# Optimization experiments

Hardware: AMD Instinct MI355X
Metric: run time of the kernel (lower is better)

## Reference

```python
import jax, jax.numpy as jnp
import numpy as np

N_NODES = 100000
N_EDGES = 1600000
IN_FEATS = 256
OUT_FEATS = 128


def setup_inputs() -> dict:
    key = jax.random.key(0)
    k1, k2, k3, k4, k5 = jax.random.split(key, 5)
    feat = jax.random.normal(k1, (N_NODES, IN_FEATS), dtype=jnp.float32)
    # xavier_uniform-like init for the weight
    limit = float(np.sqrt(6.0 / (IN_FEATS + OUT_FEATS)))
    weight = jax.random.uniform(k2, (IN_FEATS, OUT_FEATS), dtype=jnp.float32,
                                minval=-limit, maxval=limit)
    edge_weight = jax.random.uniform(k3, (N_EDGES,), dtype=jnp.float32)
    src = jax.random.randint(k4, (N_EDGES,), 0, N_NODES, dtype=jnp.int64)
    dst = jax.random.randint(k5, (N_EDGES,), 0, N_NODES, dtype=jnp.int64)
    return {"feat": feat, "weight": weight, "edge_weight": edge_weight,
            "src": src, "dst": dst}


def reference(feat, weight, edge_weight, src, dst):
    N = feat.shape[0]
    ones = jnp.ones(src.shape, dtype=feat.dtype)
    # out/in degrees from edge list (clamped to >= 1), as in DGL
    out_deg = jnp.clip(jax.ops.segment_sum(ones, src, num_segments=N), 1.0)
    in_deg = jnp.clip(jax.ops.segment_sum(ones, dst, num_segments=N), 1.0)
    # norm == 'both': pre-scale sources by out_deg^-0.5
    feat_src = feat * (out_deg ** -0.5)[:, None]
    # in_feats > out_feats branch: transform (with tanh) BEFORE aggregation
    h = jnp.tanh(feat_src @ weight)                      # [N, out]
    # message = u_mul_e: h[src] * edge_weight, then sum per destination
    m = h[src] * edge_weight[:, None]                    # [E, out]
    rst = jax.ops.segment_sum(m, dst, num_segments=N)    # [N, out]
    # norm == 'both': post-scale by in_deg^-0.5
    rst = rst * (in_deg ** -0.5)[:, None]
    return rst
```

## Files before the change

kernel.cpp:

```cpp
#include <hip/hip_runtime.h>
#include <hip/hip_fp16.h>
#include <math.h>

#define N_NODES 100000
#define N_EDGES 1600000
#define IN_F 256
#define OUT_F 128
#define SCAN_TPB 256
#define SCAN_EPB 1024

#define HR 4
#define HRANGE 25000
#define HC 64
#define HCHUNK 25000
#define PWORDS (N_NODES / 2)

#define GM_ROWS 64
#define BK 32

typedef _Float16 h8 __attribute__((ext_vector_type(8)));
typedef float f4 __attribute__((ext_vector_type(4)));
typedef int   i4v __attribute__((ext_vector_type(4)));
typedef int   i2v __attribute__((ext_vector_type(2)));
typedef float f4v __attribute__((ext_vector_type(4)));

#define GLD16(gp, lp) __builtin_amdgcn_global_load_lds( \
    (const __attribute__((address_space(1))) unsigned int*)(gp), \
    (__attribute__((address_space(3))) unsigned int*)(lp), 16, 0, 0)

__global__ __launch_bounds__(256) void hist_kernel(
        const int* __restrict__ src, const int* __restrict__ dst,
        int* __restrict__ rank, unsigned int* __restrict__ partial_in,
        unsigned int* __restrict__ partial_out) {
    __shared__ unsigned int bins[HRANGE / 2];
    int b = blockIdx.x;
    int c = b >> 3;
    int tr = b & 7;
    int type = tr >> 2;
    int r = tr & 3;
    for (int i = threadIdx.x; i < HRANGE / 2; i += 256) bins[i] = 0;
    __syncthreads();
    const int* nodes = type ? src : dst;
    const int e0 = c * HCHUNK;
    const int lo = r * HRANGE;
    const int ngroups = HCHUNK / 4;
    for (int g = threadIdx.x; g < ngroups; g += 256) {
        int e = e0 + g * 4;
        int4 n4 = *(const int4*)(nodes + e);
        int nn[4] = {n4.x, n4.y, n4.z, n4.w};
        #pragma unroll
        for (int j = 0; j < 4; ++j) {
            unsigned loc = (unsigned)(nn[j] - lo);
            if (loc < (unsigned)HRANGE) {
                unsigned sh = (loc & 1) * 16;
                unsigned old = atomicAdd(&bins[loc >> 1], 1u << sh);
                if (type == 0) rank[e + j] = (int)((old >> sh) & 0xffffu);
            }
        }
    }
    __syncthreads();
    unsigned int* part = type ? partial_out : partial_in;
    unsigned int* dstp = part + (size_t)c * PWORDS + (lo >> 1);
    for (int i = threadIdx.x; i < HRANGE / 2; i += 256) dstp[i] = bins[i];
}

__global__ __launch_bounds__(256) void fused_reduce_kernel(
        const unsigned int* __restrict__ partial_in,
        const unsigned int* __restrict__ partial_out,
        unsigned short* __restrict__ chunk_base16,
        int* __restrict__ deg_in, float* __restrict__ rs_out,
        int* __restrict__ spart, int N) {
    __shared__ int tmp[256];
    int t = threadIdx.x;
    int n0 = blockIdx.x * SCAN_EPB + t * 4;
    int run[4] = {0, 0, 0, 0};
    int sout[4] = {0, 0, 0, 0};
    if (n0 < N) {
        const int w0 = n0 >> 1;
        #pragma unroll 4
        for (int c = 0; c < HC; ++c) {
            ushort4 cb;
            cb.x = (unsigned short)run[0]; cb.y = (unsigned short)run[1];
            cb.z = (unsigned short)run[2]; cb.w = (unsigned short)run[3];
            *(ushort4*)(chunk_base16 + (size_t)c * N_NODES + n0) = cb;
            uint2 pi = *(const uint2*)(partial_in + (size_t)c * PWORDS + w0);
            run[0] += (int)(pi.x & 0xffffu);  run[1] += (int)(pi.x >> 16);
            run[2] += (int)(pi.y & 0xffffu);  run[3] += (int)(pi.y >> 16);
            uint2 po = *(const uint2*)(partial_out + (size_t)c * PWORDS + w0);
            sout[0] += (int)(po.x & 0xffffu); sout[1] += (int)(po.x >> 16);
            sout[2] += (int)(po.y & 0xffffu); sout[3] += (int)(po.y >> 16);
        }
        *(int4*)(deg_in + n0) = make_int4(run[0], run[1], run[2], run[3]);
        float4 rs;
        rs.x = rsqrtf((float)(sout[0] < 1 ? 1 : sout[0]));
        rs.y = rsqrtf((float)(sout[1] < 1 ? 1 : sout[1]));
        rs.z = rsqrtf((float)(sout[2] < 1 ? 1 : sout[2]));
        rs.w = rsqrtf((float)(sout[3] < 1 ? 1 : sout[3]));
        *(float4*)(rs_out + n0) = rs;
    }
    tmp[t] = run[0] + run[1] + run[2] + run[3];
    __syncthreads();
    for (int off = 128; off > 0; off >>= 1) {
        if (t < off) tmp[t] += tmp[t + off];
        __syncthreads();
    }
    if (t == 0) spart[blockIdx.x] = tmp[0];
}

__global__ __launch_bounds__(128) void scan_part2(const int* __restrict__ partials,
                                                  int* __restrict__ bases, int nb) {
    __shared__ int tmp[128];
    int t = threadIdx.x;
    int v = (t < nb) ? partials[t] : 0;
    tmp[t] = v;
    __syncthreads();
    int x = v;
    for (int off = 1; off < 128; off <<= 1) {
        int y = (t >= off) ? tmp[t - off] : 0;
        __syncthreads();
        x += y;
        tmp[t] = x;
        __syncthreads();
    }
    if (t < nb) bases[t] = x - v;
}

__global__ __launch_bounds__(SCAN_TPB) void scan_part3(const int* __restrict__ deg,
                                                       const int* __restrict__ bases,
                                                       int* __restrict__ row_ptr, int N) {
    __shared__ int tmp[SCAN_TPB];
    int t = threadIdx.x;
    int i0 = blockIdx.x * SCAN_EPB + t * 4;
    int v[4];
    int s = 0;
    #pragma unroll
    for (int j = 0; j < 4; ++j) { v[j] = (i0 + j < N) ? deg[i0 + j] : 0; s += v[j]; }
    tmp[t] = s;
    __syncthreads();
    int x = s;
    for (int off = 1; off < SCAN_TPB; off <<= 1) {
        int y = (t >= off) ? tmp[t - off] : 0;
        __syncthreads();
        x += y;
        tmp[t] = x;
        __syncthreads();
    }
    int excl = bases[blockIdx.x] + x - s;
    #pragma unroll
    for (int j = 0; j < 4; ++j) {
        if (i0 + j < N) row_ptr[i0 + j] = excl;
        excl += v[j];
    }
    if (blockIdx.x == gridDim.x - 1 && t == SCAN_TPB - 1) row_ptr[N] = bases[blockIdx.x] + x;
}

__global__ __launch_bounds__(256) void fill_kernel(
        const int* __restrict__ src, const int* __restrict__ dst,
        const float* __restrict__ ew, const int* __restrict__ row_ptr,
        const unsigned short* __restrict__ chunk_base16,
        const int* __restrict__ rank, int2* __restrict__ ed, int E) {
    int e0 = (blockIdx.x * 256 + threadIdx.x) * 4;
    if (e0 >= E) return;
    i4v s4 = __builtin_nontemporal_load((const i4v*)(src + e0));
    i4v d4 = __builtin_nontemporal_load((const i4v*)(dst + e0));
    f4v w4 = __builtin_nontemporal_load((const f4v*)(ew + e0));
    i4v r4 = __builtin_nontemporal_load((const i4v*)(rank + e0));
    int c = e0 / HCHUNK;
    const unsigned short* cb = chunk_base16 + (size_t)c * N_NODES;
    #pragma unroll
    for (int j = 0; j < 4; ++j) {
        int d = d4[j];
        int p = row_ptr[d] + (int)cb[d] + r4[j];
        unsigned long long v = (unsigned long long)(unsigned int)s4[j] |
                               ((unsigned long long)(unsigned int)__float_as_int(w4[j]) << 32);
        __builtin_nontemporal_store(v, (unsigned long long*)&ed[p]);
    }
}

__global__ void wt_kernel(const float* __restrict__ W, _Float16* __restrict__ Wt) {
    int i = blockIdx.x * blockDim.x + threadIdx.x;
    if (i < IN_F * OUT_F) {
        int n = i >> 8;
        int k = i & 255;
        Wt[i] = (_Float16)W[k * OUT_F + n];
    }
}

__device__ __forceinline__ float fast_tanh(float x) {
    float e = __expf(2.0f * x);
    return 1.0f - 2.0f / (e + 1.0f);
}

__global__ __launch_bounds__(256, 4) void gemm_mfma_kernel(
        const float* __restrict__ feat, const _Float16* __restrict__ Wt,
        const float* __restrict__ rs_out, __half* __restrict__ h, int N) {
    __shared__ float    a_lds[2][GM_ROWS * BK];
    __shared__ _Float16 b_lds[2][OUT_F * BK];

    const int tid  = threadIdx.x;
    const int wave = tid >> 6;
    const int lane = tid & 63;
    const int m    = lane & 15;
    const int quad = lane >> 4;
    const int n0   = wave * 32;
    const int r0   = blockIdx.x * GM_ROWS;

    const int l3 = lane >> 3;
    const int ag = (lane & 7) ^ l3;
    int arow0 = r0 + 16 * wave + l3;      if (arow0 >= N) arow0 = N - 1;
    int arow1 = r0 + 16 * wave + 8 + l3;  if (arow1 >= N) arow1 = N - 1;
    const float* ga0 = feat + (size_t)arow0 * IN_F + ag * 4;
    const float* ga1 = feat + (size_t)arow1 * IN_F + ag * 4;
    const int brow0 = 32 * wave + (lane >> 2);
    const int brow1 = 32 * wave + 16 + (lane >> 2);
    const _Float16* gb0 = Wt + (size_t)brow0 * IN_F + (lane & 3) * 8;
    const _Float16* gb1 = Wt + (size_t)brow1 * IN_F + (lane & 3) * 8;

    f4 acc[4][2];
    #pragma unroll
    for (int t = 0; t < 4; ++t) {
        acc[t][0] = (f4){0.f, 0.f, 0.f, 0.f};
        acc[t][1] = (f4){0.f, 0.f, 0.f, 0.f};
    }

    GLD16(ga0, &a_lds[0][(16 * wave) * BK]);
    GLD16(ga1, &a_lds[0][(16 * wave + 8) * BK]);
    GLD16(gb0, &b_lds[0][(32 * wave) * BK]);
    GLD16(gb1, &b_lds[0][(32 * wave + 16) * BK]);
    __syncthreads();

    #pragma unroll
    for (int kt = 0; kt < IN_F / BK; ++kt) {
        const int cb = kt & 1;
        if (kt < IN_F / BK - 1) {
            const int nb2 = cb ^ 1;
            const int ko = (kt + 1) * BK;
            GLD16(ga0 + ko, &a_lds[nb2][(16 * wave) * BK]);
            GLD16(ga1 + ko, &a_lds[nb2][(16 * wave + 8) * BK]);
            GLD16(gb0 + ko, &b_lds[nb2][(32 * wave) * BK]);
            GLD16(gb1 + ko, &b_lds[nb2][(32 * wave + 16) * BK]);
            __builtin_amdgcn_sched_barrier(0);
        }
        h8 b0 = *(const h8*)&b_lds[cb][(n0 + m) * BK + quad * 8];
        h8 b1 = *(const h8*)&b_lds[cb][(n0 + 16 + m) * BK + quad * 8];
        #pragma unroll
        for (int t = 0; t < 4; ++t) {
            const int ar = t * 16 + m;
            float4 alo = *(const float4*)&a_lds[cb][ar * BK + (((quad * 2)     ^ (m & 7)) * 4)];
            float4 ahi = *(const float4*)&a_lds[cb][ar * BK + (((quad * 2 + 1) ^ (m & 7)) * 4)];
            h8 a;
            a[0] = (_Float16)alo.x; a[1] = (_Float16)alo.y;
            a[2] = (_Float16)alo.z; a[3] = (_Float16)alo.w;
            a[4] = (_Float16)ahi.x; a[5] = (_Float16)ahi.y;
            a[6] = (_Float16)ahi.z; a[7] = (_Float16)ahi.w;
            acc[t][0] = __builtin_amdgcn_mfma_f32_16x16x32_f16(a, b0, acc[t][0], 0, 0, 0);
            acc[t][1] = __builtin_amdgcn_mfma_f32_16x16x32_f16(a, b1, acc[t][1], 0, 0, 0);
        }
        __syncthreads();
    }

    #pragma unroll
    for (int t = 0; t < 4; ++t) {
        const int crow = r0 + t * 16 + quad * 4;
        float4 rs4 = *(const float4*)&rs_out[crow];
        const float rsv[4] = {rs4.x, rs4.y, rs4.z, rs4.w};
        #pragma unroll
        for (int r = 0; r < 4; ++r) {
            const int rr = crow + r;
            if (rr < N) {
                h[(size_t)rr * OUT_F + n0 + m]      = __float2half(fast_tanh(acc[t][0][r] * rsv[r]));
                h[(size_t)rr * OUT_F + n0 + 16 + m] = __float2half(fast_tanh(acc[t][1][r] * rsv[r]));
            }
        }
    }
}

__global__ __launch_bounds__(256) void gather_kernel(
        const __half* __restrict__ h, const int2* __restrict__ ed,
        const int* __restrict__ row_ptr, float* __restrict__ out, int N) {
    int wave = threadIdx.x >> 6;
    int lane = threadIdx.x & 63;
    int node = blockIdx.x * 4 + wave;
    if (node >= N) return;
    int lo = row_ptr[node];
    int hi = row_ptr[node + 1];
    int p = lane >> 4;
    int c = lane & 15;
    float acc[4][8];
    #pragma unroll
    for (int g = 0; g < 4; ++g)
        #pragma unroll
        for (int i = 0; i < 8; ++i) acc[g][i] = 0.f;

    for (int j = lo; j < hi; j += 16) {
        i2v e[4];
        #pragma unroll
        for (int g = 0; g < 4; ++g) {
            int jj = j + g * 4 + p;
            e[g] = (jj < hi) ? __builtin_nontemporal_load((const i2v*)&ed[jj]) : (i2v){0, 0};
        }
        #pragma unroll
        for (int g = 0; g < 4; ++g) {
            float w = __int_as_float(e[g][1]);
            int4 rrow = *(const int4*)(h + (size_t)e[g][0] * OUT_F + c * 8);
            float2 t;
            t = __half22float2(*(__half2*)&rrow.x); acc[g][0] += w * t.x; acc[g][1] += w * t.y;
            t = __half22float2(*(__half2*)&rrow.y); acc[g][2] += w * t.x; acc[g][3] += w * t.y;
            t = __half22float2(*(__half2*)&rrow.z); acc[g][4] += w * t.x; acc[g][5] += w * t.y;
            t = __half22float2(*(__half2*)&rrow.w); acc[g][6] += w * t.x; acc[g][7] += w * t.y;
        }
    }
    float v[8];
    #pragma unroll
    for (int i = 0; i < 8; ++i) {
        v[i] = (acc[0][i] + acc[1][i]) + (acc[2][i] + acc[3][i]);
        v[i] += __shfl_xor(v[i], 16);
        v[i] += __shfl_xor(v[i], 32);
    }
    if (p == 0) {
        int deg = hi - lo; if (deg < 1) deg = 1;
        float rs = rsqrtf((float)deg);
        float* op = out + (size_t)node * OUT_F + c * 8;
        f4v o0 = {v[0] * rs, v[1] * rs, v[2] * rs, v[3] * rs};
        f4v o1 = {v[4] * rs, v[5] * rs, v[6] * rs, v[7] * rs};
        __builtin_nontemporal_store(o0, (f4v*)op);
        __builtin_nontemporal_store(o1, (f4v*)(op + 4));
    }
}

extern "C" void kernel_launch(void* const* d_in, const int* in_sizes, int n_in,
                              void* d_out, int out_size, void* d_ws, size_t ws_size,
                              hipStream_t stream) {
    const float* feat   = (const float*)d_in[0];
    const float* weight = (const float*)d_in[1];
    const float* ew     = (const float*)d_in[2];
    const int*   src    = (const int*)d_in[3];
    const int*   dst    = (const int*)d_in[4];
    float* out = (float*)d_out;

    char* ws = (char*)d_ws;
    float* rs_out      = (float*)(ws);
    int*   deg_in      = (int*)(ws + 400000);
    int*   row_ptr     = (int*)(ws + 800000);
    int*   spart       = (int*)(ws + 1200016);
    int*   sbases      = (int*)(ws + 1200528);
    int*   rank        = (int*)(ws + 1201056);
    unsigned int* partial_in  = (unsigned int*)(ws + 7601056);
    int2*  ed          = (int2*)(ws + 7601056);
    unsigned short* chunk_base16 = (unsigned short*)(ws + 20401056);
    unsigned int* partial_out = (unsigned int*)(ws + 33201056);
    __half* h          = (__half*)(ws + 20401056);
    _Float16* Wt       = (_Float16*)(ws + 46001056);

    const int nb = (N_NODES + SCAN_EPB - 1) / SCAN_EPB;

    hist_kernel<<<2 * HR * HC, 256, 0, stream>>>(src, dst, rank, partial_in, partial_out);
    fused_reduce_kernel<<<nb, 256, 0, stream>>>(partial_in, partial_out, chunk_base16,
                                                deg_in, rs_out, spart, N_NODES);
    scan_part2<<<1, 128, 0, stream>>>(spart, sbases, nb);
    scan_part3<<<nb, SCAN_TPB, 0, stream>>>(deg_in, sbases, row_ptr, N_NODES);
    fill_kernel<<<(N_EDGES / 4 + 255) / 256, 256, 0, stream>>>(src, dst, ew, row_ptr,
                                                               chunk_base16, rank, ed, N_EDGES);
    wt_kernel<<<(IN_F * OUT_F + 255) / 256, 256, 0, stream>>>(weight, Wt);
    gemm_mfma_kernel<<<(N_NODES + GM_ROWS - 1) / GM_ROWS, 256, 0, stream>>>(feat, Wt, rs_out, h, N_NODES);
    gather_kernel<<<(N_NODES + 3) / 4, 256, 0, stream>>>(h, ed, row_ptr, out, N_NODES);
}
```

Before: 376.8 us.

## Merge scan passes and weight transpose into neighbouring kernels, simplify gather loads

Merges the two-stage scan into one kernel in which every block redundantly scans the block partials before its local scan, and halves elements per block so nb fits in 256 threads. The weight transpose is folded into the first 128 blocks of fill_kernel. The aim is to remove two kernel launches and their serial gaps. The gather kernel also drops batched nontemporal edge loads and nontemporal output stores in favour of plain per-edge loads and stores, which may reduce load batching and memory-level parallelism.

```diff
diff --git a/kernel.cpp b/kernel.cpp
--- a/kernel.cpp
+++ b/kernel.cpp
@@ -6,8 +6,7 @@
 #define N_EDGES 1600000
 #define IN_F 256
 #define OUT_F 128
-#define SCAN_TPB 256
-#define SCAN_EPB 1024
+#define SCAN_EPB 512
 
 #define HR 4
 #define HRANGE 25000
@@ -21,7 +20,6 @@
 typedef _Float16 h8 __attribute__((ext_vector_type(8)));
 typedef float f4 __attribute__((ext_vector_type(4)));
 typedef int   i4v __attribute__((ext_vector_type(4)));
-typedef int   i2v __attribute__((ext_vector_type(2)));
 typedef float f4v __attribute__((ext_vector_type(4)));
 
 #define GLD16(gp, lp) __builtin_amdgcn_global_load_lds( \
@@ -72,33 +70,26 @@
         int* __restrict__ spart, int N) {
     __shared__ int tmp[256];
     int t = threadIdx.x;
-    int n0 = blockIdx.x * SCAN_EPB + t * 4;
-    int run[4] = {0, 0, 0, 0};
-    int sout[4] = {0, 0, 0, 0};
+    int n0 = blockIdx.x * SCAN_EPB + t * 2;
+    int run0 = 0, run1 = 0, so0 = 0, so1 = 0;
     if (n0 < N) {
         const int w0 = n0 >> 1;
         #pragma unroll 4
         for (int c = 0; c < HC; ++c) {
-            ushort4 cb;
-            cb.x = (unsigned short)run[0]; cb.y = (unsigned short)run[1];
-            cb.z = (unsigned short)run[2]; cb.w = (unsigned short)run[3];
-            *(ushort4*)(chunk_base16 + (size_t)c * N_NODES + n0) = cb;
-            uint2 pi = *(const uint2*)(partial_in + (size_t)c * PWORDS + w0);
-            run[0] += (int)(pi.x & 0xffffu);  run[1] += (int)(pi.x >> 16);
-            run[2] += (int)(pi.y & 0xffffu);  run[3] += (int)(pi.y >> 16);
-            uint2 po = *(const uint2*)(partial_out + (size_t)c * PWORDS + w0);
-            sout[0] += (int)(po.x & 0xffffu); sout[1] += (int)(po.x >> 16);
-            sout[2] += (int)(po.y & 0xffffu); sout[3] += (int)(po.y >> 16);
-        }
-        *(int4*)(deg_in + n0) = make_int4(run[0], run[1], run[2], run[3]);
-        float4 rs;
-        rs.x = rsqrtf((float)(sout[0] < 1 ? 1 : sout[0]));
-        rs.y = rsqrtf((float)(sout[1] < 1 ? 1 : sout[1]));
-        rs.z = rsqrtf((float)(sout[2] < 1 ? 1 : sout[2]));
-        rs.w = rsqrtf((float)(sout[3] < 1 ? 1 : sout[3]));
-        *(float4*)(rs_out + n0) = rs;
-    }
-    tmp[t] = run[0] + run[1] + run[2] + run[3];
+            *(unsigned int*)(chunk_base16 + (size_t)c * N_NODES + n0) =
+                (unsigned)(run0 & 0xffff) | ((unsigned)(run1 & 0xffff) << 16);
+            unsigned pi = partial_in[(size_t)c * PWORDS + w0];
+            run0 += (int)(pi & 0xffffu);  run1 += (int)(pi >> 16);
+            unsigned po = partial_out[(size_t)c * PWORDS + w0];
+            so0 += (int)(po & 0xffffu);   so1 += (int)(po >> 16);
+        }
+        *(int2*)(deg_in + n0) = make_int2(run0, run1);
+        float2 rs;
+        rs.x = rsqrtf((float)(so0 < 1 ? 1 : so0));
+        rs.y = rsqrtf((float)(so1 < 1 ? 1 : so1));
+        *(float2*)(rs_out + n0) = rs;
+    }
+    tmp[t] = run0 + run1;
     __syncthreads();
     for (int off = 128; off > 0; off >>= 1) {
         if (t < off) tmp[t] += tmp[t + off];
@@ -107,58 +98,56 @@
     if (t == 0) spart[blockIdx.x] = tmp[0];
 }
 
-__global__ __launch_bounds__(128) void scan_part2(const int* __restrict__ partials,
-                                                  int* __restrict__ bases, int nb) {
-    __shared__ int tmp[128];
+__global__ __launch_bounds__(256) void scan_kernel(const int* __restrict__ deg,
+                                                   const int* __restrict__ spart,
+                                                   int* __restrict__ row_ptr, int N, int nb) {
+    __shared__ int sp[256];
+    __shared__ int tmp[256];
     int t = threadIdx.x;
-    int v = (t < nb) ? partials[t] : 0;
-    tmp[t] = v;
-    __syncthreads();
-    int x = v;
-    for (int off = 1; off < 128; off <<= 1) {
+    int pv = (t < nb) ? spart[t] : 0;
+    sp[t] = pv;
+    __syncthreads();
+    int x = pv;
+    for (int off = 1; off < 256; off <<= 1) {
+        int y = (t >= off) ? sp[t - off] : 0;
+        __syncthreads();
+        x += y;
+        sp[t] = x;
+        __syncthreads();
+    }
+    const int base = (blockIdx.x == 0) ? 0 : sp[blockIdx.x - 1];
+    if (blockIdx.x == 0 && t == 0) row_ptr[N] = sp[nb - 1];
+    int i0 = blockIdx.x * SCAN_EPB + t * 2;
+    int v0 = (i0 < N) ? deg[i0] : 0;
+    int v1 = (i0 + 1 < N) ? deg[i0 + 1] : 0;
+    int s = v0 + v1;
+    tmp[t] = s;
+    __syncthreads();
+    int x2 = s;
+    for (int off = 1; off < 256; off <<= 1) {
         int y = (t >= off) ? tmp[t - off] : 0;
         __syncthreads();
-        x += y;
-        tmp[t] = x;
-        __syncthreads();
-    }
-    if (t < nb) bases[t] = x - v;
-}
-
-__global__ __launch_bounds__(SCAN_TPB) void scan_part3(const int* __restrict__ deg,
-                                                       const int* __restrict__ bases,
-                                                       int* __restrict__ row_ptr, int N) {
-    __shared__ int tmp[SCAN_TPB];
-    int t = threadIdx.x;
-    int i0 = blockIdx.x * SCAN_EPB + t * 4;
-    int v[4];
-    int s = 0;
-    #pragma unroll
-    for (int j = 0; j < 4; ++j) { v[j] = (i0 + j < N) ? deg[i0 + j] : 0; s += v[j]; }
-    tmp[t] = s;
-    __syncthreads();
-    int x = s;
-    for (int off = 1; off < SCAN_TPB; off <<= 1) {
-        int y = (t >= off) ? tmp[t - off] : 0;
-        __syncthreads();
-        x += y;
-        tmp[t] = x;
-        __syncthreads();
-    }
-    int excl = bases[blockIdx.x] + x - s;
-    #pragma unroll
-    for (int j = 0; j < 4; ++j) {
-        if (i0 + j < N) row_ptr[i0 + j] = excl;
-        excl += v[j];
-    }
-    if (blockIdx.x == gridDim.x - 1 && t == SCAN_TPB - 1) row_ptr[N] = bases[blockIdx.x] + x;
+        x2 += y;
+        tmp[t] = x2;
+        __syncthreads();
+    }
+    int excl = base + x2 - s;
+    if (i0 < N)     row_ptr[i0]     = excl;
+    if (i0 + 1 < N) row_ptr[i0 + 1] = excl + v0;
 }
 
 __global__ __launch_bounds__(256) void fill_kernel(
         const int* __restrict__ src, const int* __restrict__ dst,
         const float* __restrict__ ew, const int* __restrict__ row_ptr,
         const unsigned short* __restrict__ chunk_base16,
-        const int* __restrict__ rank, int2* __restrict__ ed, int E) {
+        const int* __restrict__ rank, int2* __restrict__ ed,
+        const float* __restrict__ W, _Float16* __restrict__ Wt, int E) {
+    if (blockIdx.x < 128) {
+        int i = blockIdx.x * 256 + threadIdx.x;
+        int n = i >> 8;
+        int k = i & 255;
+        Wt[i] = (_Float16)W[k * OUT_F + n];
+    }
     int e0 = (blockIdx.x * 256 + threadIdx.x) * 4;
     if (e0 >= E) return;
     i4v s4 = __builtin_nontemporal_load((const i4v*)(src + e0));
@@ -174,15 +163,6 @@
         unsigned long long v = (unsigned long long)(unsigned int)s4[j] |
                                ((unsigned long long)(unsigned int)__float_as_int(w4[j]) << 32);
         __builtin_nontemporal_store(v, (unsigned long long*)&ed[p]);
-    }
-}
-
-__global__ void wt_kernel(const float* __restrict__ W, _Float16* __restrict__ Wt) {
-    int i = blockIdx.x * blockDim.x + threadIdx.x;
-    if (i < IN_F * OUT_F) {
-        int n = i >> 8;
-        int k = i & 255;
-        Wt[i] = (_Float16)W[k * OUT_F + n];
     }
 }
 
@@ -293,16 +273,12 @@
         for (int i = 0; i < 8; ++i) acc[g][i] = 0.f;
 
     for (int j = lo; j < hi; j += 16) {
-        i2v e[4];
         #pragma unroll
         for (int g = 0; g < 4; ++g) {
             int jj = j + g * 4 + p;
-            e[g] = (jj < hi) ? __builtin_nontemporal_load((const i2v*)&ed[jj]) : (i2v){0, 0};
-        }
-        #pragma unroll
-        for (int g = 0; g < 4; ++g) {
-            float w = __int_as_float(e[g][1]);
-            int4 rrow = *(const int4*)(h + (size_t)e[g][0] * OUT_F + c * 8);
+            int2 e = (jj < hi) ? ed[jj] : make_int2(0, 0);
+            float w = __int_as_float(e.y);
+            int4 rrow = *(const int4*)(h + (size_t)e.x * OUT_F + c * 8);
             float2 t;
             t = __half22float2(*(__half2*)&rrow.x); acc[g][0] += w * t.x; acc[g][1] += w * t.y;
             t = __half22float2(*(__half2*)&rrow.y); acc[g][2] += w * t.x; acc[g][3] += w * t.y;
@@ -321,10 +297,8 @@
         int deg = hi - lo; if (deg < 1) deg = 1;
         float rs = rsqrtf((float)deg);
         float* op = out + (size_t)node * OUT_F + c * 8;
-        f4v o0 = {v[0] * rs, v[1] * rs, v[2] * rs, v[3] * rs};
-        f4v o1 = {v[4] * rs, v[5] * rs, v[6] * rs, v[7] * rs};
-        __builtin_nontemporal_store(o0, (f4v*)op);
-        __builtin_nontemporal_store(o1, (f4v*)(op + 4));
+        *(float4*)op       = make_float4(v[0] * rs, v[1] * rs, v[2] * rs, v[3] * rs);
+        *(float4*)(op + 4) = make_float4(v[4] * rs, v[5] * rs, v[6] * rs, v[7] * rs);
     }
 }
 
@@ -343,7 +317,6 @@
     int*   deg_in      = (int*)(ws + 400000);
     int*   row_ptr     = (int*)(ws + 800000);
     int*   spart       = (int*)(ws + 1200016);
-    int*   sbases      = (int*)(ws + 1200528);
     int*   rank        = (int*)(ws + 1201056);
     unsigned int* partial_in  = (unsigned int*)(ws + 7601056);
     int2*  ed          = (int2*)(ws + 7601056);
@@ -357,11 +330,10 @@
     hist_kernel<<<2 * HR * HC, 256, 0, stream>>>(src, dst, rank, partial_in, partial_out);
     fused_reduce_kernel<<<nb, 256, 0, stream>>>(partial_in, partial_out, chunk_base16,
                                                 deg_in, rs_out, spart, N_NODES);
-    scan_part2<<<1, 128, 0, stream>>>(spart, sbases, nb);
-    scan_part3<<<nb, SCAN_TPB, 0, stream>>>(deg_in, sbases, row_ptr, N_NODES);
+    scan_kernel<<<nb, 256, 0, stream>>>(deg_in, spart, row_ptr, N_NODES, nb);
     fill_kernel<<<(N_EDGES / 4 + 255) / 256, 256, 0, stream>>>(src, dst, ew, row_ptr,
-                                                               chunk_base16, rank, ed, N_EDGES);
-    wt_kernel<<<(IN_F * OUT_F + 255) / 256, 256, 0, stream>>>(weight, Wt);
+                                                               chunk_base16, rank, ed,
+                                                               weight, Wt, N_EDGES);
     gemm_mfma_kernel<<<(N_NODES + GM_ROWS - 1) / GM_ROWS, 256, 0, stream>>>(feat, Wt, rs_out, h, N_NODES);
     gather_kernel<<<(N_NODES + 3) / 4, 256, 0, stream>>>(h, ed, row_ptr, out, N_NODES);
 }
```

New measurement: 372.7 us. No clear change (-1.1%).
